# Performance work log

Measured on AMD Instinct MI355X. Metric: run time of the kernel, lower is better.

## Reference

```python
import jax, jax.numpy as jnp
import numpy as np

N_NODES = 100000
N_EDGES = 1600000
K = 4
D = 16  # d_in // K
NEG_SLOPE = 0.01  # F.leaky_relu default
EPS = 1e-12       # F.normalize default eps


def setup_inputs() -> dict:
    key = jax.random.key(0)
    k1, k2, k3 = jax.random.split(key, 3)
    f_in = jax.random.normal(k1, (N_NODES, K, D), dtype=jnp.float32)
    edges = jax.random.randint(k2, (N_EDGES, 2), 0, N_NODES, dtype=jnp.int64)
    attn_w = jax.random.normal(k3, (K, 2 * D), dtype=jnp.float32) * 0.1
    return {"f_in": f_in, "edges": edges, "attn_w": attn_w}


def reference(f_in, edges, attn_w):
    # f_in: [N, K, D], edges: [E, 2] (src, dst), attn_w: [K, 2D]
    src = edges[:, 0]
    dst = edges[:, 1]
    f_src = f_in[src]            # [E, K, D] gather
    f_dst = f_in[dst]            # [E, K, D] gather
    f_edge = jnp.concatenate([f_src, f_dst], axis=2)  # [E, K, 2D]
    # per-factor attention score + leaky_relu
    score = jnp.einsum('ekd,kd->ek', f_edge, attn_w)  # [E, K]
    score = jnp.where(score >= 0, score, NEG_SLOPE * score)
    # scatter_softmax over edges grouped by src, per factor
    smax = jax.ops.segment_max(score, src, num_segments=N_NODES)  # [N, K]
    smax = jnp.where(jnp.isfinite(smax), smax, 0.0)  # empty segments -> -inf -> 0
    ex = jnp.exp(score - smax[src])                               # [E, K]
    denom = jax.ops.segment_sum(ex, src, num_segments=N_NODES)    # [N, K]
    norm = ex / denom[src]                                        # [E, K]
    # weighted scatter_add of neighbor embeddings
    m = jax.ops.segment_sum(f_dst * norm[:, :, None], src, num_segments=N_NODES)  # [N, K, D]
    # F.normalize(m): L2 over dim=1 (factor axis)
    l2 = jnp.sqrt(jnp.sum(m * m, axis=1, keepdims=True))  # [N, 1, D]
    return m / jnp.maximum(l2, EPS)
```

## Files before the change

kernel.cpp:

```cpp
#include <hip/hip_runtime.h>

#define N_NODES 100000
#define N_EDGES 1600000
#define KH 4
#define DH 16
#define KD (KH * DH)
#define MAXDEG 64
#define NEG_SLOPE 0.01f

#define T 256
#define SCORE_BLOCKS ((N_NODES * KH + T - 1) / T)
#define SCATTER_BLOCKS ((N_EDGES + T - 1) / T)

__device__ __forceinline__ float lrelu(float x) {
    return (x >= 0.f) ? x : NEG_SLOPE * x;
}

__global__ void k_pre(const float* __restrict__ f_in,
                      const float* __restrict__ attn_w,
                      const int* __restrict__ edges,
                      float* __restrict__ a_src,
                      float* __restrict__ a_dst,
                      int* __restrict__ deg,
                      int* __restrict__ dst_pad) {
    if (blockIdx.x < SCORE_BLOCKS) {
        int i = blockIdx.x * T + threadIdx.x;
        if (i >= N_NODES * KH) return;
        int k = i & (KH - 1);
        const float4* f  = (const float4*)(f_in + (size_t)i * DH);
        const float4* w1 = (const float4*)(attn_w + k * 2 * DH);
        const float4* w2 = (const float4*)(attn_w + k * 2 * DH + DH);
        float s1 = 0.f, s2 = 0.f;
#pragma unroll
        for (int j = 0; j < DH / 4; ++j) {
            float4 fv = f[j];
            float4 av = w1[j];
            float4 bv = w2[j];
            s1 += fv.x * av.x + fv.y * av.y + fv.z * av.z + fv.w * av.w;
            s2 += fv.x * bv.x + fv.y * bv.y + fv.z * bv.z + fv.w * bv.w;
        }
        a_src[i] = s1;
        a_dst[i] = s2;
    } else {
        int e = (blockIdx.x - SCORE_BLOCKS) * T + threadIdx.x;
        if (e >= N_EDGES) return;
        int2 sd = ((const int2*)edges)[e];
        int pos = atomicAdd(&deg[sd.x], 1);
        if (pos < MAXDEG)
            dst_pad[(size_t)sd.x * MAXDEG + pos] = sd.y;
    }
}

__global__ void k_node_aggregate(const int* __restrict__ deg,
                                 const int* __restrict__ dst_pad,
                                 const float* __restrict__ a_src,
                                 const float* __restrict__ a_dst,
                                 const float* __restrict__ f_in,
                                 float* __restrict__ out) {
    int gid  = blockIdx.x * blockDim.x + threadIdx.x;
    int n    = gid >> 6;
    int lane = gid & 63;
    if (n >= N_NODES) return;
    int k = lane >> 4;

    int dg = deg[n];
    if (dg > MAXDEG) dg = MAXDEG;
    float as = a_src[n * KH + k];
    const int* dl = dst_pad + (size_t)n * MAXDEG;

    float acc = 0.f, dsum = 0.f;
    int i = 0;
    int dg4 = dg & ~3;
    for (; i < dg4; i += 4) {
        int4 d4 = *(const int4*)(dl + i);
        float a0 = a_dst[d4.x * KH + k];
        float a1 = a_dst[d4.y * KH + k];
        float a2 = a_dst[d4.z * KH + k];
        float a3 = a_dst[d4.w * KH + k];
        float f0 = f_in[(size_t)d4.x * KD + lane];
        float f1 = f_in[(size_t)d4.y * KD + lane];
        float f2 = f_in[(size_t)d4.z * KD + lane];
        float f3 = f_in[(size_t)d4.w * KD + lane];
        float e0 = __expf(lrelu(as + a0));
        float e1 = __expf(lrelu(as + a1));
        float e2 = __expf(lrelu(as + a2));
        float e3 = __expf(lrelu(as + a3));
        dsum += (e0 + e1) + (e2 + e3);
        acc  += e0 * f0 + e1 * f1 + e2 * f2 + e3 * f3;
    }
    for (; i < dg; ++i) {
        int d = dl[i];
        float ex = __expf(lrelu(as + a_dst[d * KH + k]));
        dsum += ex;
        acc  += ex * f_in[(size_t)d * KD + lane];
    }

    float v = (dsum > 0.f) ? (acc / dsum) : 0.f;
    float ss = v * v;
    ss += __shfl_xor(ss, 16);
    ss += __shfl_xor(ss, 32);
    float inv = 1.f / fmaxf(sqrtf(ss), 1e-12f);
    out[(size_t)n * KD + lane] = v * inv;
}

extern "C" void kernel_launch(void* const* d_in, const int* in_sizes, int n_in,
                              void* d_out, int out_size, void* d_ws, size_t ws_size,
                              hipStream_t stream) {
    const float* f_in   = (const float*)d_in[0];
    const int*   edges  = (const int*)d_in[1];
    const float* attn_w = (const float*)d_in[2];
    float* out = (float*)d_out;

    float* a_src  = (float*)d_ws;
    float* a_dst  = a_src + N_NODES * KH;
    int*   deg    = (int*)(a_dst + N_NODES * KH);
    int*   dst_pad= deg + N_NODES;

    hipMemsetAsync(deg, 0, (size_t)N_NODES * sizeof(int), stream);

    k_pre<<<SCORE_BLOCKS + SCATTER_BLOCKS, T, 0, stream>>>(f_in, attn_w, edges,
                                                           a_src, a_dst, deg, dst_pad);
    long long total = (long long)N_NODES * 64;
    k_node_aggregate<<<(int)((total + T - 1) / T), T, 0, stream>>>(deg, dst_pad, a_src, a_dst,
                                                                   f_in, out);
}
```

Measured before the change: 271.1 us.

## Partition edge scatter and aggregation by node range for XCD-local L2 reuse

The edge scatter is split into 8 node partitions. Each block group reads every edge but only handles sources inside its partition, and the round-robin block index (blockIdx & 7) probably lines each partition up with one XCD so that atomics and dst_pad writes stay in one L2. The aggregation kernel maps blocks to nodes the same way, and its neighbour loop is unrolled to 8 gathers for more memory-level parallelism. The cost is that every edge is read 8 times, using nontemporal loads, and the speedup depends on the block-to-XCD mapping.

New measurement: 237.4 us. 12.4% less time.

```diff
diff --git a/kernel.cpp b/kernel.cpp
--- a/kernel.cpp
+++ b/kernel.cpp
@@ -9,8 +9,12 @@
 #define NEG_SLOPE 0.01f
 
 #define T 256
-#define SCORE_BLOCKS ((N_NODES * KH + T - 1) / T)
-#define SCATTER_BLOCKS ((N_EDGES + T - 1) / T)
+#define NPART 8
+#define PART_SZ ((N_NODES + NPART - 1) / NPART)
+#define SCORE_BLOCKS 1568
+#define SCATTER_PB 256
+#define SCATTER_BLOCKS (SCATTER_PB * NPART)
+#define AGG_BLOCKS ((PART_SZ / 4) * NPART)
 
 __device__ __forceinline__ float lrelu(float x) {
     return (x >= 0.f) ? x : NEG_SLOPE * x;
@@ -42,12 +46,31 @@
         a_src[i] = s1;
         a_dst[i] = s2;
     } else {
-        int e = (blockIdx.x - SCORE_BLOCKS) * T + threadIdx.x;
-        if (e >= N_EDGES) return;
-        int2 sd = ((const int2*)edges)[e];
-        int pos = atomicAdd(&deg[sd.x], 1);
-        if (pos < MAXDEG)
-            dst_pad[(size_t)sd.x * MAXDEG + pos] = sd.y;
+        int sb = blockIdx.x - SCORE_BLOCKS;
+        int p  = sb & (NPART - 1);
+        int q  = sb >> 3;
+        int lo = p * PART_SZ;
+        int hi = lo + PART_SZ;
+        const long long* e2 = (const long long*)edges;
+        const int npair = N_EDGES / 2;
+        for (int i = q * T + threadIdx.x; i < npair; i += SCATTER_PB * T) {
+            long long v0 = __builtin_nontemporal_load(&e2[2 * i]);
+            long long v1 = __builtin_nontemporal_load(&e2[2 * i + 1]);
+            int s0 = (int)(v0 & 0xffffffffLL);
+            int d0 = (int)(v0 >> 32);
+            int s1 = (int)(v1 & 0xffffffffLL);
+            int d1 = (int)(v1 >> 32);
+            if (s0 >= lo && s0 < hi) {
+                int pos = atomicAdd(&deg[s0], 1);
+                if (pos < MAXDEG)
+                    dst_pad[(size_t)s0 * MAXDEG + pos] = d0;
+            }
+            if (s1 >= lo && s1 < hi) {
+                int pos = atomicAdd(&deg[s1], 1);
+                if (pos < MAXDEG)
+                    dst_pad[(size_t)s1 * MAXDEG + pos] = d1;
+            }
+        }
     }
 }
 
@@ -57,9 +80,11 @@
                                  const float* __restrict__ a_dst,
                                  const float* __restrict__ f_in,
                                  float* __restrict__ out) {
-    int gid  = blockIdx.x * blockDim.x + threadIdx.x;
-    int n    = gid >> 6;
-    int lane = gid & 63;
+    int p    = blockIdx.x & (NPART - 1);
+    int q    = blockIdx.x >> 3;
+    int wid  = threadIdx.x >> 6;
+    int lane = threadIdx.x & 63;
+    int n    = p * PART_SZ + q * 4 + wid;
     if (n >= N_NODES) return;
     int k = lane >> 4;
 
@@ -70,23 +95,37 @@
 
     float acc = 0.f, dsum = 0.f;
     int i = 0;
-    int dg4 = dg & ~3;
-    for (; i < dg4; i += 4) {
-        int4 d4 = *(const int4*)(dl + i);
-        float a0 = a_dst[d4.x * KH + k];
-        float a1 = a_dst[d4.y * KH + k];
-        float a2 = a_dst[d4.z * KH + k];
-        float a3 = a_dst[d4.w * KH + k];
-        float f0 = f_in[(size_t)d4.x * KD + lane];
-        float f1 = f_in[(size_t)d4.y * KD + lane];
-        float f2 = f_in[(size_t)d4.z * KD + lane];
-        float f3 = f_in[(size_t)d4.w * KD + lane];
+    int dg8 = dg & ~7;
+    for (; i < dg8; i += 8) {
+        int4 da = *(const int4*)(dl + i);
+        int4 db = *(const int4*)(dl + i + 4);
+        float a0 = a_dst[da.x * KH + k];
+        float a1 = a_dst[da.y * KH + k];
+        float a2 = a_dst[da.z * KH + k];
+        float a3 = a_dst[da.w * KH + k];
+        float a4 = a_dst[db.x * KH + k];
+        float a5 = a_dst[db.y * KH + k];
+        float a6 = a_dst[db.z * KH + k];
+        float a7 = a_dst[db.w * KH + k];
+        float f0 = f_in[(size_t)da.x * KD + lane];
+        float f1 = f_in[(size_t)da.y * KD + lane];
+        float f2 = f_in[(size_t)da.z * KD + lane];
+        float f3 = f_in[(size_t)da.w * KD + lane];
+        float f4 = f_in[(size_t)db.x * KD + lane];
+        float f5 = f_in[(size_t)db.y * KD + lane];
+        float f6 = f_in[(size_t)db.z * KD + lane];
+        float f7 = f_in[(size_t)db.w * KD + lane];
         float e0 = __expf(lrelu(as + a0));
         float e1 = __expf(lrelu(as + a1));
         float e2 = __expf(lrelu(as + a2));
         float e3 = __expf(lrelu(as + a3));
-        dsum += (e0 + e1) + (e2 + e3);
-        acc  += e0 * f0 + e1 * f1 + e2 * f2 + e3 * f3;
+        float e4 = __expf(lrelu(as + a4));
+        float e5 = __expf(lrelu(as + a5));
+        float e6 = __expf(lrelu(as + a6));
+        float e7 = __expf(lrelu(as + a7));
+        dsum += ((e0 + e1) + (e2 + e3)) + ((e4 + e5) + (e6 + e7));
+        acc  += e0 * f0 + e1 * f1 + e2 * f2 + e3 * f3
+              + e4 * f4 + e5 * f5 + e6 * f6 + e7 * f7;
     }
     for (; i < dg; ++i) {
         int d = dl[i];
@@ -116,11 +155,9 @@
     int*   deg    = (int*)(a_dst + N_NODES * KH);
     int*   dst_pad= deg + N_NODES;
 
-    hipMemsetAsync(deg, 0, (size_t)N_NODES * sizeof(int), stream);
+    (void)hipMemsetAsync(deg, 0, (size_t)N_NODES * sizeof(int), stream);
 
     k_pre<<<SCORE_BLOCKS + SCATTER_BLOCKS, T, 0, stream>>>(f_in, attn_w, edges,
                                                            a_src, a_dst, deg, dst_pad);
-    long long total = (long long)N_NODES * 64;
-    k_node_aggregate<<<(int)((total + T - 1) / T), T, 0, stream>>>(deg, dst_pad, a_src, a_dst,
-                                                                   f_in, out);
+    k_node_aggregate<<<AGG_BLOCKS, T, 0, stream>>>(deg, dst_pad, a_src, a_dst, f_in, out);
 }
```
